# Kernel tuning notes

Hardware: AMD Instinct MI355X
Metric: run time of the kernel (lower is better)

## Reference

```python
import jax, jax.numpy as jnp
import numpy as np

N_NODES = 100000
HIDDEN = 128
E = 524288  # edges per graph (pos and neg)


def setup_inputs() -> dict:
    key = jax.random.key(0)
    ks = jax.random.split(key, 8)
    return {
        "z_src": jax.random.normal(ks[0], (N_NODES, HIDDEN), dtype=jnp.float32),
        "z_dst": jax.random.normal(ks[1], (N_NODES, HIDDEN), dtype=jnp.float32),
        "pos_src": jax.random.randint(ks[2], (E,), 0, N_NODES, dtype=jnp.int64),
        "pos_dst": jax.random.randint(ks[3], (E,), 0, N_NODES, dtype=jnp.int64),
        "neg_src": jax.random.randint(ks[4], (E,), 0, N_NODES, dtype=jnp.int64),
        "neg_dst": jax.random.randint(ks[5], (E,), 0, N_NODES, dtype=jnp.int64),
        "W1": jax.random.normal(ks[6], (2 * HIDDEN, HIDDEN), dtype=jnp.float32) * (1.0 / np.sqrt(2 * HIDDEN)),
        "b1": jnp.zeros((HIDDEN,), dtype=jnp.float32),
        "W2": jax.random.normal(ks[7], (HIDDEN, 1), dtype=jnp.float32) * (1.0 / np.sqrt(HIDDEN)),
        "b2": jnp.zeros((1,), dtype=jnp.float32),
    }


def reference(z_src, z_dst, pos_src, pos_dst, neg_src, neg_dst, W1, b1, W2, b2):
    # Gather endpoint features for pos then neg edges (cat along edge dim)
    src_idx = jnp.concatenate([pos_src, neg_src])  # [2E]
    dst_idx = jnp.concatenate([pos_dst, neg_dst])  # [2E]
    z = jnp.concatenate([z_src[src_idx], z_dst[dst_idx]], axis=-1)  # [2E, 2h]
    z = jax.nn.relu(z @ W1 + b1)  # [2E, h]
    z = z @ W2 + b2               # [2E, 1]
    return z.reshape(-1)
```

## Files before the change

### kernel.cpp

```cpp
#include <hip/hip_runtime.h>
#include <hip/hip_bf16.h>
#include <cstdint>

#define N_NODES 100000
#define HIDDEN  128
#define NEDGE   524288
#define NT      6250
#define PBLK    256
#define WSTRIDE (PBLK * 4)

typedef __attribute__((ext_vector_type(8))) short short8;
typedef __attribute__((ext_vector_type(4))) float f32x4;

__device__ __forceinline__ unsigned short f2b(float f) {
    unsigned u = __float_as_uint(f);
    u += 0x7FFFu + ((u >> 16) & 1u);
    return (unsigned short)(u >> 16);
}
__device__ __forceinline__ float b2f(unsigned x16) {
    return __uint_as_float(x16 << 16);
}

__device__ __forceinline__ void async_copy16(const float* g, float* l) {
    __builtin_amdgcn_global_load_lds(
        (const __attribute__((address_space(1))) unsigned int*)g,
        (__attribute__((address_space(3))) unsigned int*)l,
        16, 0, 0);
}

__global__ void wp_kernel(const float* __restrict__ W1,
                          unsigned short* __restrict__ Wp)
{
    const int f = blockIdx.x;
    const int tb = blockIdx.y;
    const int lane = threadIdx.x;
    const int t = lane & 15, q = lane >> 4;
    const int n = f >> 2, ks = f & 3;
    short8 v;
#pragma unroll
    for (int j = 0; j < 8; ++j)
        v[j] = (short)f2b(W1[(size_t)(tb * 128 + ks * 32 + q * 8 + j) * 128 + n * 16 + t]);
    *(short8*)(Wp + ((size_t)(tb * 32 + f) * 64 + lane) * 8) = v;
}

__global__ __launch_bounds__(256, 2)
void precompute_kernel(const float* __restrict__ z_src,
                       const float* __restrict__ z_dst,
                       const unsigned short* __restrict__ Wp,
                       unsigned short* __restrict__ Asrc,
                       unsigned short* __restrict__ Adst)
{
    const int table = blockIdx.y;
    const float* __restrict__ z = table ? z_dst : z_src;
    unsigned short* __restrict__ A = table ? Adst : Asrc;

    __shared__ float zbuf[4][2][2048];

    const int tid = threadIdx.x;
    const int wave = tid >> 6;
    const int lane = tid & 63;
    const int t = lane & 15;
    const int q = lane >> 4;

    short8 wfrag[32];
    {
        const unsigned short* wp = Wp + ((size_t)table * 32 * 64 + lane) * 8;
#pragma unroll
        for (int f = 0; f < 32; ++f)
            wfrag[f] = *(const short8*)(wp + (size_t)f * 64 * 8);
    }

    const int lhi = lane >> 5;
    const int llo = lane & 31;
#define STAGE(m0, p)                                                          \
    do {                                                                      \
        _Pragma("unroll")                                                     \
        for (int j = 0; j < 8; ++j) {                                         \
            const int r = j * 2 + lhi;                                        \
            const int c = llo ^ (r & 7);                                      \
            async_copy16(z + (size_t)((m0) + r) * 128 + c * 4,                \
                         &zbuf[wave][p][j * 256]);                            \
        }                                                                     \
    } while (0)

    int tile = blockIdx.x * 4 + wave;
    int p = 0;
    STAGE(tile * 16, 0);
    __builtin_amdgcn_s_waitcnt(0xF70);
    asm volatile("" ::: "memory");

    while (tile < NT) {
        const int m0 = tile * 16;
        const int ntile = tile + WSTRIDE;
        const int nm0 = (ntile < NT ? ntile : tile) * 16;
        STAGE(nm0, p ^ 1);
        asm volatile("" ::: "memory");
        __builtin_amdgcn_s_waitcnt(0xF78);
        asm volatile("" ::: "memory");

        short8 b[4];
#pragma unroll
        for (int ks = 0; ks < 4; ++ks) {
            const int c0 = ks * 8 + 2 * q;
            const int s = t & 7;
            const float4 v0 = *(const float4*)&zbuf[wave][p][(t * 32 + (c0 ^ s)) * 4];
            const float4 v1 = *(const float4*)&zbuf[wave][p][(t * 32 + ((c0 + 1) ^ s)) * 4];
            b[ks][0] = (short)f2b(v0.x); b[ks][1] = (short)f2b(v0.y);
            b[ks][2] = (short)f2b(v0.z); b[ks][3] = (short)f2b(v0.w);
            b[ks][4] = (short)f2b(v1.x); b[ks][5] = (short)f2b(v1.y);
            b[ks][6] = (short)f2b(v1.z); b[ks][7] = (short)f2b(v1.w);
        }

        f32x4 acc[8];
#pragma unroll
        for (int n = 0; n < 8; ++n) acc[n] = (f32x4){0.f, 0.f, 0.f, 0.f};
#pragma unroll
        for (int n = 0; n < 8; ++n)
#pragma unroll
            for (int ks = 0; ks < 4; ++ks)
                acc[n] = __builtin_amdgcn_mfma_f32_16x16x32_bf16(
                             wfrag[n * 4 + ks], b[ks], acc[n], 0, 0, 0);

        unsigned short* arow = A + (size_t)(m0 + t) * 128;
#pragma unroll
        for (int n = 0; n < 8; ++n) {
            ushort4 h;
            h.x = f2b(acc[n][0]); h.y = f2b(acc[n][1]);
            h.z = f2b(acc[n][2]); h.w = f2b(acc[n][3]);
            *(ushort4*)(arow + n * 16 + q * 4) = h;
        }

        p ^= 1;
        tile = ntile;
    }
#undef STAGE
}

__global__ __launch_bounds__(256, 4)
void edge_kernel(const unsigned short* __restrict__ Asrc,
                 const unsigned short* __restrict__ Adst,
                 const int* __restrict__ pos_src,
                 const int* __restrict__ pos_dst,
                 const int* __restrict__ neg_src,
                 const int* __restrict__ neg_dst,
                 const float* __restrict__ b1,
                 const float* __restrict__ W2,
                 const float* __restrict__ b2,
                 float* __restrict__ out)
{
    const int tid = threadIdx.x;
    const int t = tid & 15;
    const int g = tid >> 4;

    const bool is_pos = blockIdx.x < 4096;
    const int* __restrict__ sp = is_pos ? pos_src : neg_src;
    const int* __restrict__ dp = is_pos ? pos_dst : neg_dst;
    const int eb = (is_pos ? blockIdx.x : blockIdx.x - 4096) * 128;

    float b1r[8], w2r[8];
#pragma unroll
    for (int j = 0; j < 8; ++j) {
        b1r[j] = b1[t * 8 + j];
        w2r[j] = W2[t * 8 + j];
    }
    const float bias2 = b2[0];

    int sidx[8], didx[8];
#pragma unroll
    for (int i = 0; i < 8; ++i) {
        sidx[i] = sp[eb + i * 16 + g];
        didx[i] = dp[eb + i * 16 + g];
    }

    uint4 ua[8], ub[8];
#pragma unroll
    for (int i = 0; i < 8; ++i) {
        ua[i] = *(const uint4*)(Asrc + (size_t)sidx[i] * 128 + t * 8);
        ub[i] = *(const uint4*)(Adst + (size_t)didx[i] * 128 + t * 8);
    }

#pragma unroll
    for (int i = 0; i < 8; ++i) {
        float acc = 0.f;
        const unsigned* pa = (const unsigned*)&ua[i];
        const unsigned* pb = (const unsigned*)&ub[i];
#pragma unroll
        for (int j2 = 0; j2 < 4; ++j2) {
            float h0 = b2f(pa[j2] & 0xFFFFu) + b2f(pb[j2] & 0xFFFFu) + b1r[2 * j2];
            float h1 = b2f(pa[j2] >> 16)     + b2f(pb[j2] >> 16)     + b1r[2 * j2 + 1];
            h0 = fmaxf(h0, 0.f);
            h1 = fmaxf(h1, 0.f);
            acc = fmaf(h0, w2r[2 * j2], acc);
            acc = fmaf(h1, w2r[2 * j2 + 1], acc);
        }
        acc += __shfl_xor(acc, 1);
        acc += __shfl_xor(acc, 2);
        acc += __shfl_xor(acc, 4);
        acc += __shfl_xor(acc, 8);
        if (t == 0) out[blockIdx.x * 128 + i * 16 + g] = acc + bias2;
    }
}

extern "C" void kernel_launch(void* const* d_in, const int* in_sizes, int n_in,
                              void* d_out, int out_size, void* d_ws, size_t ws_size,
                              hipStream_t stream) {
    const float* z_src  = (const float*)d_in[0];
    const float* z_dst  = (const float*)d_in[1];
    const int* pos_src  = (const int*)d_in[2];
    const int* pos_dst  = (const int*)d_in[3];
    const int* neg_src  = (const int*)d_in[4];
    const int* neg_dst  = (const int*)d_in[5];
    const float* W1     = (const float*)d_in[6];
    const float* b1     = (const float*)d_in[7];
    const float* W2     = (const float*)d_in[8];
    const float* b2     = (const float*)d_in[9];
    float* out = (float*)d_out;

    unsigned short* Asrc = (unsigned short*)d_ws;
    unsigned short* Adst = Asrc + (size_t)N_NODES * HIDDEN;
    unsigned short* Wp   = Adst + (size_t)N_NODES * HIDDEN;

    wp_kernel<<<dim3(32, 2), 64, 0, stream>>>(W1, Wp);

    precompute_kernel<<<dim3(PBLK, 2), 256, 0, stream>>>(z_src, z_dst, Wp,
                                                         Asrc, Adst);

    edge_kernel<<<8192, 256, 0, stream>>>(Asrc, Adst, pos_src, pos_dst,
                                          neg_src, neg_dst, b1, W2, b2, out);
}
```

Measured before the change: 222.4 us.

## Fold bias into precompute, stage output via LDS, double-buffer edge gathers

The precompute kernel now adds b1 into the src-table projection and writes each output tile through a swizzled LDS buffer, so the global stores become row-contiguous 16-byte writes instead of scattered 8-byte writes. The edge kernel drops the per-edge bias add and gathers rows in a two-deep software pipeline of two edges per stage instead of loading all eight up front. This cuts register use so launch bounds can rise to 6 blocks per SIMD for more occupancy. Risks: reusing the z staging buffer for output could race with the next async prefetch into the other buffer, and fewer loads in flight per thread may reduce memory-level parallelism.

Measured after the change: 222.3 us. No clear change (-0.0%).

```diff
diff --git a/kernel.cpp b/kernel.cpp
--- a/kernel.cpp
+++ b/kernel.cpp
@@ -47,6 +47,7 @@
 void precompute_kernel(const float* __restrict__ z_src,
                        const float* __restrict__ z_dst,
                        const unsigned short* __restrict__ Wp,
+                       const float* __restrict__ b1,
                        unsigned short* __restrict__ Asrc,
                        unsigned short* __restrict__ Adst)
 {
@@ -69,6 +70,12 @@
         for (int f = 0; f < 32; ++f)
             wfrag[f] = *(const short8*)(wp + (size_t)f * 64 * 8);
     }
+
+    float4 b1v[8];
+#pragma unroll
+    for (int n = 0; n < 8; ++n)
+        b1v[n] = (table == 0) ? *(const float4*)(b1 + n * 16 + q * 4)
+                              : make_float4(0.f, 0.f, 0.f, 0.f);
 
     const int lhi = lane >> 5;
     const int llo = lane & 31;
@@ -121,14 +128,25 @@
                 acc[n] = __builtin_amdgcn_mfma_f32_16x16x32_bf16(
                              wfrag[n * 4 + ks], b[ks], acc[n], 0, 0, 0);
 
-        unsigned short* arow = A + (size_t)(m0 + t) * 128;
+        unsigned short* ob = (unsigned short*)&zbuf[wave][p][0];
+        const int sw = (t & 7) * 2;
 #pragma unroll
         for (int n = 0; n < 8; ++n) {
             ushort4 h;
-            h.x = f2b(acc[n][0]); h.y = f2b(acc[n][1]);
-            h.z = f2b(acc[n][2]); h.w = f2b(acc[n][3]);
-            *(ushort4*)(arow + n * 16 + q * 4) = h;
-        }
+            h.x = f2b(acc[n][0] + b1v[n].x);
+            h.y = f2b(acc[n][1] + b1v[n].y);
+            h.z = f2b(acc[n][2] + b1v[n].z);
+            h.w = f2b(acc[n][3] + b1v[n].w);
+            *(ushort4*)&ob[t * 136 + (((n * 4 + q) ^ sw) * 4)] = h;
+        }
+        const int rr = lane >> 4;
+#pragma unroll
+        for (int it = 0; it < 4; ++it) {
+            const int r = it * 4 + rr;
+            const uint4 v = *(const uint4*)&ob[r * 136 + (((2 * t) ^ ((r & 7) * 2)) * 4)];
+            *(uint4*)(A + (size_t)(m0 + r) * 128 + t * 8) = v;
+        }
+        asm volatile("" ::: "memory");
 
         p ^= 1;
         tile = ntile;
@@ -136,14 +154,13 @@
 #undef STAGE
 }
 
-__global__ __launch_bounds__(256, 4)
+__global__ __launch_bounds__(256, 6)
 void edge_kernel(const unsigned short* __restrict__ Asrc,
                  const unsigned short* __restrict__ Adst,
                  const int* __restrict__ pos_src,
                  const int* __restrict__ pos_dst,
                  const int* __restrict__ neg_src,
                  const int* __restrict__ neg_dst,
-                 const float* __restrict__ b1,
                  const float* __restrict__ W2,
                  const float* __restrict__ b2,
                  float* __restrict__ out)
@@ -155,14 +172,11 @@
     const bool is_pos = blockIdx.x < 4096;
     const int* __restrict__ sp = is_pos ? pos_src : neg_src;
     const int* __restrict__ dp = is_pos ? pos_dst : neg_dst;
-    const int eb = (is_pos ? blockIdx.x : blockIdx.x - 4096) * 128;
-
-    float b1r[8], w2r[8];
-#pragma unroll
-    for (int j = 0; j < 8; ++j) {
-        b1r[j] = b1[t * 8 + j];
-        w2r[j] = W2[t * 8 + j];
-    }
+    const int eb = (is_pos ? (int)blockIdx.x : (int)blockIdx.x - 4096) * 128;
+
+    float w2r[8];
+#pragma unroll
+    for (int j = 0; j < 8; ++j) w2r[j] = W2[t * 8 + j];
     const float bias2 = b2[0];
 
     int sidx[8], didx[8];
@@ -172,32 +186,46 @@
         didx[i] = dp[eb + i * 16 + g];
     }
 
-    uint4 ua[8], ub[8];
-#pragma unroll
-    for (int i = 0; i < 8; ++i) {
-        ua[i] = *(const uint4*)(Asrc + (size_t)sidx[i] * 128 + t * 8);
-        ub[i] = *(const uint4*)(Adst + (size_t)didx[i] * 128 + t * 8);
-    }
-
-#pragma unroll
-    for (int i = 0; i < 8; ++i) {
-        float acc = 0.f;
-        const unsigned* pa = (const unsigned*)&ua[i];
-        const unsigned* pb = (const unsigned*)&ub[i];
-#pragma unroll
-        for (int j2 = 0; j2 < 4; ++j2) {
-            float h0 = b2f(pa[j2] & 0xFFFFu) + b2f(pb[j2] & 0xFFFFu) + b1r[2 * j2];
-            float h1 = b2f(pa[j2] >> 16)     + b2f(pb[j2] >> 16)     + b1r[2 * j2 + 1];
-            h0 = fmaxf(h0, 0.f);
-            h1 = fmaxf(h1, 0.f);
-            acc = fmaf(h0, w2r[2 * j2], acc);
-            acc = fmaf(h1, w2r[2 * j2 + 1], acc);
-        }
-        acc += __shfl_xor(acc, 1);
-        acc += __shfl_xor(acc, 2);
-        acc += __shfl_xor(acc, 4);
-        acc += __shfl_xor(acc, 8);
-        if (t == 0) out[blockIdx.x * 128 + i * 16 + g] = acc + bias2;
+    uint4 ua[2][2], ub[2][2];
+#pragma unroll
+    for (int k = 0; k < 2; ++k) {
+        ua[0][k] = *(const uint4*)(Asrc + (size_t)sidx[k] * 128 + t * 8);
+        ub[0][k] = *(const uint4*)(Adst + (size_t)didx[k] * 128 + t * 8);
+    }
+    asm volatile("" ::: "memory");
+
+#pragma unroll
+    for (int c = 0; c < 4; ++c) {
+        if (c < 3) {
+#pragma unroll
+            for (int k = 0; k < 2; ++k) {
+                ua[(c + 1) & 1][k] =
+                    *(const uint4*)(Asrc + (size_t)sidx[(c + 1) * 2 + k] * 128 + t * 8);
+                ub[(c + 1) & 1][k] =
+                    *(const uint4*)(Adst + (size_t)didx[(c + 1) * 2 + k] * 128 + t * 8);
+            }
+        }
+        asm volatile("" ::: "memory");
+#pragma unroll
+        for (int k = 0; k < 2; ++k) {
+            const unsigned* pa = (const unsigned*)&ua[c & 1][k];
+            const unsigned* pb = (const unsigned*)&ub[c & 1][k];
+            float acc = 0.f;
+#pragma unroll
+            for (int j2 = 0; j2 < 4; ++j2) {
+                float h0 = b2f(pa[j2] & 0xFFFFu) + b2f(pb[j2] & 0xFFFFu);
+                float h1 = b2f(pa[j2] >> 16)     + b2f(pb[j2] >> 16);
+                h0 = fmaxf(h0, 0.f);
+                h1 = fmaxf(h1, 0.f);
+                acc = fmaf(h0, w2r[2 * j2], acc);
+                acc = fmaf(h1, w2r[2 * j2 + 1], acc);
+            }
+            acc += __shfl_xor(acc, 1);
+            acc += __shfl_xor(acc, 2);
+            acc += __shfl_xor(acc, 4);
+            acc += __shfl_xor(acc, 8);
+            if (t == 0) out[blockIdx.x * 128 + (c * 2 + k) * 16 + g] = acc + bias2;
+        }
     }
 }
 
@@ -222,9 +250,9 @@
 
     wp_kernel<<<dim3(32, 2), 64, 0, stream>>>(W1, Wp);
 
-    precompute_kernel<<<dim3(PBLK, 2), 256, 0, stream>>>(z_src, z_dst, Wp,
+    precompute_kernel<<<dim3(PBLK, 2), 256, 0, stream>>>(z_src, z_dst, Wp, b1,
                                                          Asrc, Adst);
 
     edge_kernel<<<8192, 256, 0, stream>>>(Asrc, Adst, pos_src, pos_dst,
-                                          neg_src, neg_dst, b1, W2, b2, out);
-}
+                                          neg_src, neg_dst, W2, b2, out);
+}
```
